# Optimization experiments

Measured on AMD Instinct MI355X. Metric: run time of the kernel, lower is better.

## Reference

```python
import jax, jax.numpy as jnp
import numpy as np

DECAY = 0.99
EPS = 1e-05


def setup_inputs() -> dict:
    key = jax.random.key(0)
    k1, k2, k3 = jax.random.split(key, 3)
    N, K, D = 131072, 1024, 64
    return {
        "z": jax.random.normal(k1, (N, D), dtype=jnp.float32),
        "embeddings": jax.random.normal(k2, (K, D), dtype=jnp.float32),
        "cluster_size": jnp.ones((K,), dtype=jnp.float32),
        "ema_embed_sum": jax.random.normal(k3, (K, D), dtype=jnp.float32),
    }


def reference(z, embeddings, cluster_size, ema_embed_sum):
    # z: [N, D]; embeddings/ema_embed_sum: [K, D]; cluster_size: [K]
    N, D = z.shape
    K = embeddings.shape[0]

    # squared pairwise distances via the ||a||^2 - 2ab + ||b||^2 expansion
    d = (
        jnp.sum(z * z, axis=-1, keepdims=True)
        - 2.0 * (z @ embeddings.T)
        + jnp.sum(embeddings * embeddings, axis=-1)
    )  # [N, K]
    encoding_indices = jnp.argmin(d, axis=1)  # [N]
    z_q = embeddings[encoding_indices]  # [N, D]

    # EMA codebook update (training mode; one_hot.sum(0) == counts, one_hot.T @ z == segment_sum)
    counts = jax.ops.segment_sum(jnp.ones((N,), z.dtype), encoding_indices, num_segments=K)
    new_cluster_size = cluster_size * DECAY + (1.0 - DECAY) * counts
    embed_sum = jax.ops.segment_sum(z, encoding_indices, num_segments=K)  # [K, D]
    new_ema_embed_sum = ema_embed_sum * DECAY + (1.0 - DECAY) * embed_sum
    n = jnp.sum(new_cluster_size)
    cs = (new_cluster_size + EPS) / (n + K * EPS) * n
    new_embeddings = new_ema_embed_sum / cs[:, None]

    commitment_loss = jnp.mean((z - z_q) ** 2)
    z_q_st = z + jax.lax.stop_gradient(z_q - z)  # value == z_q
    return (z_q_st, commitment_loss, encoding_indices, new_embeddings, new_cluster_size, new_ema_embed_sum)
```

## Files before the change

kernel.cpp:

```cpp
#include <hip/hip_runtime.h>

#define N_PTS 131072
#define K_CODES 1024
#define DIM 64
#define DECAYF 0.99f
#define OMDF 0.01f
#define EPSF 1e-5f

#define OUT_ZQ      0
#define OUT_LOSS    8388608
#define OUT_IDX     8388609
#define OUT_NEWEMB  8519681
#define OUT_NEWCS   8585217
#define OUT_NEWEMA  8586241

#define WS_C8       0
#define WS_ACNT     8192
#define WS_LOSS     8208
#define WS_EMBSUM   8224
#define WS_ZERO_END 73760
#define WS_ENORM    73760
#define WS_CUR8     74784
#define WS_CS       82976
#define WS_AMBIG    84000
#define WS_ORDER    215072
#define WS_E2S      215072

#define STEP_BYTES  16640
#define STEP_SHORTS 8320
#define STEP_FLOATS 4160

typedef __attribute__((ext_vector_type(8))) short bf16x8;
typedef __attribute__((ext_vector_type(4))) float f32x4;

static __device__ inline short f2bf(float f) {
    unsigned u = __float_as_uint(f);
    unsigned r = (u + 0x7fffu + ((u >> 16) & 1u)) >> 16;
    return (short)r;
}
static __device__ inline float bf2f(short h) {
    return __uint_as_float(((unsigned)(unsigned short)h) << 16);
}

static __device__ __forceinline__ void gload16(const char* g, char* l) {
    __builtin_amdgcn_global_load_lds(
        (const __attribute__((address_space(1))) void*)g,
        (__attribute__((address_space(3))) void*)l, 16, 0, 0);
}
static __device__ __forceinline__ void gload4(const char* g, char* l) {
    __builtin_amdgcn_global_load_lds(
        (const __attribute__((address_space(1))) void*)g,
        (__attribute__((address_space(3))) void*)l, 4, 0, 0);
}

__global__ __launch_bounds__(256) void econv_kernel(const float* __restrict__ E,
                                                    short* __restrict__ E2S,
                                                    float* __restrict__ enorm) {
    int tid = threadIdx.x;
    int code = blockIdx.x * 64 + (tid >> 2);
    int seg = tid & 3;
    const float4* e4 = (const float4*)(E + (size_t)code * DIM + seg * 16);
    float4 v0 = e4[0], v1 = e4[1], v2 = e4[2], v3 = e4[3];
    float f[16];
    f[0]=v0.x; f[1]=v0.y; f[2]=v0.z; f[3]=v0.w;
    f[4]=v1.x; f[5]=v1.y; f[6]=v1.z; f[7]=v1.w;
    f[8]=v2.x; f[9]=v2.y; f[10]=v2.z; f[11]=v2.w;
    f[12]=v3.x; f[13]=v3.y; f[14]=v3.z; f[15]=v3.w;
    float s = 0.f;
#pragma unroll
    for (int j = 0; j < 16; ++j) s += f[j] * f[j];
    s += __shfl_xor(s, 1);
    s += __shfl_xor(s, 2);
    short hi[16], lo[16];
#pragma unroll
    for (int j = 0; j < 16; ++j) {
        float m = -2.f * f[j];
        short h = f2bf(m);
        hi[j] = h;
        lo[j] = f2bf(m - bf2f(h));
    }
    int sstep = code >> 6;
    int tau = (code >> 4) & 3;
    int cc = code & 15;
    size_t stepb = (size_t)sstep * STEP_SHORTS;
    int p_hi = seg >> 1, p_lo = 2 + (seg >> 1);
#pragma unroll
    for (int h8 = 0; h8 < 2; ++h8) {
        int qq = ((seg & 1) << 1) | h8;
        size_t base = stepb + tau * 2048 + qq * 128 + cc * 8;
        bf16x8 vh, vl;
#pragma unroll
        for (int j = 0; j < 8; ++j) { vh[j] = hi[h8 * 8 + j]; vl[j] = lo[h8 * 8 + j]; }
        *(bf16x8*)(E2S + base + p_hi * 512) = vh;
        *(bf16x8*)(E2S + base + p_lo * 512) = vl;
    }
    if (seg == 0) {
        ((float*)E2S)[(size_t)sstep * STEP_FLOATS + 4096 + tau * 16 + cc] = s;
        enorm[code] = s;
    }
}

__global__ __launch_bounds__(256) void argmin_mfma(const float* __restrict__ z,
                                                   const short* __restrict__ E2S,
                                                   float* __restrict__ out_idx_f,
                                                   float* __restrict__ counts8,
                                                   int* __restrict__ ambig_cnt,
                                                   int* __restrict__ ambig,
                                                   float* __restrict__ loss_ws) {
    int tid = threadIdx.x;
    int w = tid >> 6, lane = tid & 63;
    int c = lane & 15, q = lane >> 4;
    int mbase = blockIdx.x * 256 + w * 64;

    __shared__ char smem[2 * STEP_BYTES] __attribute__((aligned(16)));
    const char* E2Sc = (const char*)E2S;

#define STAGE(SBUF, SSTEP) do {                                               \
    const char* g_ = E2Sc + (size_t)(SSTEP) * STEP_BYTES + w * 1024 + lane * 16; \
    char* l_ = smem + (SBUF) * STEP_BYTES + w * 1024;                         \
    gload16(g_,          l_);                                                 \
    gload16(g_ + 4096,   l_ + 4096);                                          \
    gload16(g_ + 8192,   l_ + 8192);                                          \
    gload16(g_ + 12288,  l_ + 12288);                                         \
    if (w == 0)                                                               \
        gload4(E2Sc + (size_t)(SSTEP) * STEP_BYTES + 16384 + lane * 4,        \
               smem + (SBUF) * STEP_BYTES + 16384);                           \
} while (0)

    STAGE(0, 0);

    bf16x8 a[4][4];
    float znorm_t[4];
#pragma unroll
    for (int t = 0; t < 4; ++t) {
        const float* zp = z + (size_t)(mbase + t * 16 + c) * DIM;
        const float4* z4a = (const float4*)(zp + q * 8);
        const float4* z4b = (const float4*)(zp + 32 + q * 8);
        float f[16];
        float4 v0 = z4a[0], v1 = z4a[1], v2 = z4b[0], v3 = z4b[1];
        f[0]=v0.x; f[1]=v0.y; f[2]=v0.z; f[3]=v0.w;
        f[4]=v1.x; f[5]=v1.y; f[6]=v1.z; f[7]=v1.w;
        f[8]=v2.x; f[9]=v2.y; f[10]=v2.z; f[11]=v2.w;
        f[12]=v3.x; f[13]=v3.y; f[14]=v3.z; f[15]=v3.w;
        float zn = 0.f;
#pragma unroll
        for (int j = 0; j < 16; ++j) zn += f[j] * f[j];
#pragma unroll
        for (int off = 16; off < 64; off <<= 1) zn += __shfl_xor(zn, off);
        znorm_t[t] = zn;
#pragma unroll
        for (int j = 0; j < 8; ++j) {
            short h0 = f2bf(f[j]);
            a[t][0][j] = h0;
            a[t][2][j] = f2bf(f[j] - bf2f(h0));
            short h1 = f2bf(f[8 + j]);
            a[t][1][j] = h1;
            a[t][3][j] = f2bf(f[8 + j] - bf2f(h1));
        }
    }

    float s1[16], s2[16];
#pragma unroll
    for (int idx = 0; idx < 16; ++idx) { s1[idx] = INFINITY; s2[idx] = INFINITY; }

    __syncthreads();

    int bfr = (q << 4) + c;
    for (int st = 0; st < 16; ++st) {
        if (st < 15) STAGE((st + 1) & 1, st + 1);
        const short* lb = (const short*)(smem + (st & 1) * STEP_BYTES);
        const float* lef = (const float*)(smem + (st & 1) * STEP_BYTES + 16384);
#pragma unroll
        for (int tau = 0; tau < 4; ++tau) {
            const bf16x8* bp = (const bf16x8*)lb + tau * 256 + bfr;
            bf16x8 bh0 = bp[0], bh1 = bp[64], bl0 = bp[128], bl1 = bp[192];
            float en = lef[tau * 16 + c];
            unsigned vcode = (unsigned)((((st << 2) + tau) << 4) | c);
#pragma unroll
            for (int t = 0; t < 4; ++t) {
                f32x4 acc = {en, en, en, en};
                acc = __builtin_amdgcn_mfma_f32_16x16x32_bf16(a[t][0], bl0, acc, 0, 0, 0);
                acc = __builtin_amdgcn_mfma_f32_16x16x32_bf16(a[t][1], bl1, acc, 0, 0, 0);
                acc = __builtin_amdgcn_mfma_f32_16x16x32_bf16(a[t][2], bh0, acc, 0, 0, 0);
                acc = __builtin_amdgcn_mfma_f32_16x16x32_bf16(a[t][3], bh1, acc, 0, 0, 0);
                acc = __builtin_amdgcn_mfma_f32_16x16x32_bf16(a[t][0], bh0, acc, 0, 0, 0);
                acc = __builtin_amdgcn_mfma_f32_16x16x32_bf16(a[t][1], bh1, acc, 0, 0, 0);
#pragma unroll
                for (int i = 0; i < 4; ++i) {
                    float sp = __uint_as_float(
                        (__float_as_uint(acc[i]) & 0xFFFFFC00u) | vcode);
                    int idx = t * 4 + i;
                    float ns2 = __builtin_amdgcn_fmed3f(s1[idx], s2[idx], sp);
                    s1[idx] = fminf(s1[idx], sp);
                    s2[idx] = ns2;
                }
            }
        }
        __syncthreads();
    }
#undef STAGE

#pragma unroll
    for (int off = 1; off < 16; off <<= 1) {
#pragma unroll
        for (int idx = 0; idx < 16; ++idx) {
            float os1 = __shfl_xor(s1[idx], off);
            float os2 = __shfl_xor(s2[idx], off);
            float ns1 = fminf(s1[idx], os1);
            s2[idx] = fminf(fmaxf(s1[idx], os1), fminf(s2[idx], os2));
            s1[idx] = ns1;
        }
    }

    float znr[16];
#pragma unroll
    for (int t = 0; t < 4; ++t)
#pragma unroll
        for (int i = 0; i < 4; ++i)
            znr[t * 4 + i] = __shfl(znorm_t[t], (q << 4) | (q * 4 + i), 64);

    __shared__ float lred[16];
    float lsum = 0.f;
    if (c == 0) {
#pragma unroll
        for (int idx = 0; idx < 16; ++idx) {
            int t = idx >> 2, i = idx & 3;
            int row = mbase + t * 16 + q * 4 + i;
            unsigned b1 = __float_as_uint(s1[idx]);
            int code = (int)(b1 & 1023u);
            out_idx_f[row] = (float)code;
            float s1v = __uint_as_float(b1 & 0xFFFFFC00u);
            float gap = s2[idx] - s1[idx];
            float tau = 0.008f + 8e-4f * (fabsf(s1[idx]) + fabsf(s2[idx]));
            if (gap >= tau) {
                atomicAdd(&counts8[(((unsigned)row >> 8) & 7) * K_CODES + code], 1.0f);
                lsum += znr[idx] + s1v;
            } else {
                int p = atomicAdd(ambig_cnt, 1);
                ambig[p] = row;
            }
        }
        lred[w * 4 + q] = lsum;
    }
    __syncthreads();
    if (tid == 0) {
        float tot = 0.f;
#pragma unroll
        for (int i = 0; i < 16; ++i) tot += lred[i];
        atomicAdd(loss_ws, tot);
    }
}

__global__ __launch_bounds__(256) void rescue_kernel(const float* __restrict__ z,
                                                     const float* __restrict__ E,
                                                     const float* __restrict__ enorm,
                                                     const int* __restrict__ ambig_cnt,
                                                     const int* __restrict__ ambig,
                                                     float* __restrict__ out_idx_f,
                                                     float* __restrict__ counts8,
                                                     float* __restrict__ loss_ws) {
    int lane = threadIdx.x & 63;
    int wave = (blockIdx.x * 256 + threadIdx.x) >> 6;
    int nw = gridDim.x * 4;
    int cnt = *ambig_cnt;
    for (int a = 2 * wave; a < cnt; a += 2 * nw) {
        int row0 = ambig[a];
        bool two = (a + 1) < cnt;
        int row1 = two ? ambig[a + 1] : row0;
        const float4* zp0 = (const float4*)(z + (size_t)row0 * DIM);
        const float4* zp1 = (const float4*)(z + (size_t)row1 * DIM);
        float4 zr0[16], zr1[16];
        float zn0 = 0.f, zn1 = 0.f;
#pragma unroll
        for (int i = 0; i < 16; ++i) {
            float4 u = zp0[i], v = zp1[i];
            zr0[i] = u; zr1[i] = v;
            zn0 += u.x * u.x + u.y * u.y + u.z * u.z + u.w * u.w;
            zn1 += v.x * v.x + v.y * v.y + v.z * v.z + v.w * v.w;
        }
        float best0 = INFINITY, best1 = INFINITY;
        int bi0 = 0, bi1 = 0;
        for (int j = 0; j < 16; ++j) {
            int code = j * 64 + lane;
            const float4* ep = (const float4*)(E + (size_t)code * DIM);
            float a0 = 0.f, a1 = 0.f, a2 = 0.f, a3 = 0.f;
            float c0 = 0.f, c1 = 0.f, c2 = 0.f, c3 = 0.f;
#pragma unroll
            for (int i = 0; i < 16; ++i) {
                float4 ev = ep[i];
                a0 += zr0[i].x * ev.x; a1 += zr0[i].y * ev.y;
                a2 += zr0[i].z * ev.z; a3 += zr0[i].w * ev.w;
                c0 += zr1[i].x * ev.x; c1 += zr1[i].y * ev.y;
                c2 += zr1[i].z * ev.z; c3 += zr1[i].w * ev.w;
            }
            float en = enorm[code];
            float s0 = en - 2.f * ((a0 + a1) + (a2 + a3));
            float s1 = en - 2.f * ((c0 + c1) + (c2 + c3));
            if (s0 < best0) { best0 = s0; bi0 = code; }
            if (s1 < best1) { best1 = s1; bi1 = code; }
        }
#pragma unroll
        for (int off = 1; off < 64; off <<= 1) {
            float ob = __shfl_xor(best0, off);
            int oi = __shfl_xor(bi0, off);
            if (ob < best0 || (ob == best0 && oi < bi0)) { best0 = ob; bi0 = oi; }
            float ob1 = __shfl_xor(best1, off);
            int oi1 = __shfl_xor(bi1, off);
            if (ob1 < best1 || (ob1 == best1 && oi1 < bi1)) { best1 = ob1; bi1 = oi1; }
        }
        if (lane == 0) {
            out_idx_f[row0] = (float)bi0;
            atomicAdd(&counts8[(((unsigned)row0 >> 8) & 7) * K_CODES + bi0], 1.0f);
            float ladd = zn0 + best0;
            if (two) {
                out_idx_f[row1] = (float)bi1;
                atomicAdd(&counts8[(((unsigned)row1 >> 8) & 7) * K_CODES + bi1], 1.0f);
                ladd += zn1 + best1;
            }
            atomicAdd(loss_ws, ladd);
        }
    }
}

__global__ __launch_bounds__(1024) void scan_kernel(const float* __restrict__ cluster_size,
                                                    const float* __restrict__ counts8,
                                                    float* __restrict__ ncs_out,
                                                    float* __restrict__ cs_ws,
                                                    int* __restrict__ cursor8) {
    int k = threadIdx.x;
    int lane = k & 63, wv = k >> 6;
    float c8[8];
    float cnt = 0.f;
#pragma unroll
    for (int s = 0; s < 8; ++s) { c8[s] = counts8[s * K_CODES + k]; cnt += c8[s]; }
    float ncs = cluster_size[k] * DECAYF + OMDF * cnt;
    ncs_out[k] = ncs;

    int v = (int)cnt;
    int vs = v;
#pragma unroll
    for (int off = 1; off < 64; off <<= 1) {
        int o = __shfl_up(vs, off, 64);
        if (lane >= off) vs += o;
    }
    float fs = ncs;
#pragma unroll
    for (int off = 1; off < 64; off <<= 1) fs += __shfl_xor(fs, off);

    __shared__ int wtot[16];
    __shared__ float ftot[16];
    __shared__ float nsh;
    if (lane == 63) wtot[wv] = vs;
    if (lane == 0) ftot[wv] = fs;
    __syncthreads();
    if (k == 0) {
        int run = 0; float fn = 0.f;
#pragma unroll
        for (int i = 0; i < 16; ++i) {
            int t = wtot[i]; wtot[i] = run; run += t;
            fn += ftot[i];
        }
        nsh = fn;
    }
    __syncthreads();
    float n = nsh;
    cs_ws[k] = (ncs + EPSF) / (n + (float)K_CODES * EPSF) * n;

    int excl = vs - v + wtot[wv];
    int run = excl;
#pragma unroll
    for (int s = 0; s < 8; ++s) { cursor8[s * K_CODES + k] = run; run += (int)c8[s]; }
}

__global__ __launch_bounds__(256) void scatter_zq_kernel(const float* __restrict__ E,
                                                         const float* __restrict__ idx_f,
                                                         int* __restrict__ cursor8,
                                                         int* __restrict__ order,
                                                         float* __restrict__ zq) {
    __shared__ int s_k[256];
    int tid = threadIdx.x;
    int rbase = blockIdx.x * 256;
    int row = rbase + tid;
    int k = (int)idx_f[row];
    s_k[tid] = k;
    int shard = ((unsigned)row >> 8) & 7;
    int p = atomicAdd(&cursor8[shard * K_CODES + k], 1);
    order[p] = (k << 17) | row;
    __syncthreads();
    size_t ebase = (size_t)rbase * DIM;
#pragma unroll 4
    for (int it = 0; it < 64; ++it) {
        int le = it * 256 + tid;
        int rl = le >> 6, d = le & 63;
        zq[ebase + le] = E[(size_t)s_k[rl] * DIM + d];
    }
}

__global__ __launch_bounds__(256) void segsum_kernel(const float* __restrict__ z,
                                                     const int* __restrict__ order,
                                                     float* __restrict__ embsum) {
    int lane = threadIdx.x & 63;
    int w = threadIdx.x >> 6;
    int wave = blockIdx.x * 4 + w;
    int base = wave * 64;

    int my = order[base + lane];

    int cur = __shfl(my, 0, 64) >> 17;
    float sum = 0.f;
#pragma unroll 8
    for (int i = 0; i < 64; ++i) {
        int p = __shfl(my, i, 64);
        int row = p & 0x1FFFF;
        int code = p >> 17;
        float v = z[(size_t)row * DIM + lane];
        if (code != cur) {
            atomicAdd(&embsum[(size_t)cur * DIM + lane], sum);
            sum = 0.f;
            cur = code;
        }
        sum += v;
    }
    atomicAdd(&embsum[(size_t)cur * DIM + lane], sum);
}

__global__ __launch_bounds__(256) void ema2_kernel(const float* __restrict__ ema,
                                                   const float* __restrict__ embsum,
                                                   const float* __restrict__ cs_ws,
                                                   const float* __restrict__ loss_ws,
                                                   float* __restrict__ newema_out,
                                                   float* __restrict__ newemb_out,
                                                   float* __restrict__ loss_out) {
    int i = blockIdx.x * 256 + threadIdx.x;
    float nes = ema[i] * DECAYF + OMDF * embsum[i];
    newema_out[i] = nes;
    newemb_out[i] = nes / cs_ws[i >> 6];
    if (i == 0)
        loss_out[0] = loss_ws[0] * (1.0f / ((float)N_PTS * (float)DIM));
}

extern "C" void kernel_launch(void* const* d_in, const int* in_sizes, int n_in,
                              void* d_out, int out_size, void* d_ws, size_t ws_size,
                              hipStream_t stream) {
    const float* z            = (const float*)d_in[0];
    const float* E            = (const float*)d_in[1];
    const float* cluster_size = (const float*)d_in[2];
    const float* ema          = (const float*)d_in[3];
    float* out = (float*)d_out;
    float* ws  = (float*)d_ws;

    hipMemsetAsync(ws, 0, (size_t)WS_ZERO_END * sizeof(float), stream);

    econv_kernel<<<K_CODES / 64, 256, 0, stream>>>(E, (short*)(ws + WS_E2S),
                                                   ws + WS_ENORM);

    argmin_mfma<<<N_PTS / 256, 256, 0, stream>>>(z, (const short*)(ws + WS_E2S),
                                                 out + OUT_IDX,
                                                 ws + WS_C8,
                                                 (int*)(ws + WS_ACNT),
                                                 (int*)(ws + WS_AMBIG),
                                                 ws + WS_LOSS);

    rescue_kernel<<<512, 256, 0, stream>>>(z, E, ws + WS_ENORM,
                                           (const int*)(ws + WS_ACNT),
                                           (const int*)(ws + WS_AMBIG),
                                           out + OUT_IDX,
                                           ws + WS_C8,
                                           ws + WS_LOSS);

    scan_kernel<<<1, 1024, 0, stream>>>(cluster_size, ws + WS_C8,
                                        out + OUT_NEWCS, ws + WS_CS,
                                        (int*)(ws + WS_CUR8));

    scatter_zq_kernel<<<N_PTS / 256, 256, 0, stream>>>(E, out + OUT_IDX,
                                                       (int*)(ws + WS_CUR8),
                                                       (int*)(ws + WS_ORDER),
                                                       out + OUT_ZQ);

    segsum_kernel<<<N_PTS / 256, 256, 0, stream>>>(z,
                                                   (const int*)(ws + WS_ORDER),
                                                   ws + WS_EMBSUM);

    ema2_kernel<<<K_CODES * DIM / 256, 256, 0, stream>>>(ema, ws + WS_EMBSUM,
                                                         ws + WS_CS,
                                                         ws + WS_LOSS,
                                                         out + OUT_NEWEMA,
                                                         out + OUT_NEWEMB,
                                                         out + OUT_LOSS);
}
```

Before: 224.3 us.

## Fuse tail kernels into one persistent kernel with grid barriers

Merges the rescue, scan, z_q scatter, segment-sum and EMA kernels into a single persistent launch of 256 blocks that separates its phases with software grid barriers. The workspace memset moves into the codebook conversion kernel, and the argmin kernel's reduction buffer now reuses existing shared memory. The aim is to remove several launches and their gaps on the stream. In exchange, the scatter and segsum phases run on fewer blocks with grid-stride loops, and the spin barrier relies on all 256 blocks being resident at once.

```diff
diff --git a/kernel.cpp b/kernel.cpp
--- a/kernel.cpp
+++ b/kernel.cpp
@@ -6,6 +6,8 @@
 #define DECAYF 0.99f
 #define OMDF 0.01f
 #define EPSF 1e-5f
+
+#define TAIL_BLKS 256
 
 #define OUT_ZQ      0
 #define OUT_LOSS    8388608
@@ -54,9 +56,13 @@
 }
 
 __global__ __launch_bounds__(256) void econv_kernel(const float* __restrict__ E,
-                                                    short* __restrict__ E2S,
-                                                    float* __restrict__ enorm) {
+                                                    float* __restrict__ ws) {
     int tid = threadIdx.x;
+    int gid = blockIdx.x * 256 + tid;
+    for (int i = gid; i < WS_ZERO_END; i += 16 * 256) ws[i] = 0.f;
+
+    short* E2S = (short*)(ws + WS_E2S);
+    float* enorm = ws + WS_ENORM;
     int code = blockIdx.x * 64 + (tid >> 2);
     int seg = tid & 3;
     const float4* e4 = (const float4*)(E + (size_t)code * DIM + seg * 16);
@@ -219,7 +225,7 @@
         for (int i = 0; i < 4; ++i)
             znr[t * 4 + i] = __shfl(znorm_t[t], (q << 4) | (q * 4 + i), 64);
 
-    __shared__ float lred[16];
+    float* lred = (float*)smem;
     float lsum = 0.f;
     if (c == 0) {
 #pragma unroll
@@ -251,192 +257,216 @@
     }
 }
 
-__global__ __launch_bounds__(256) void rescue_kernel(const float* __restrict__ z,
-                                                     const float* __restrict__ E,
-                                                     const float* __restrict__ enorm,
-                                                     const int* __restrict__ ambig_cnt,
-                                                     const int* __restrict__ ambig,
-                                                     float* __restrict__ out_idx_f,
-                                                     float* __restrict__ counts8,
-                                                     float* __restrict__ loss_ws) {
-    int lane = threadIdx.x & 63;
-    int wave = (blockIdx.x * 256 + threadIdx.x) >> 6;
-    int nw = gridDim.x * 4;
-    int cnt = *ambig_cnt;
-    for (int a = 2 * wave; a < cnt; a += 2 * nw) {
-        int row0 = ambig[a];
-        bool two = (a + 1) < cnt;
-        int row1 = two ? ambig[a + 1] : row0;
-        const float4* zp0 = (const float4*)(z + (size_t)row0 * DIM);
-        const float4* zp1 = (const float4*)(z + (size_t)row1 * DIM);
-        float4 zr0[16], zr1[16];
-        float zn0 = 0.f, zn1 = 0.f;
-#pragma unroll
-        for (int i = 0; i < 16; ++i) {
-            float4 u = zp0[i], v = zp1[i];
-            zr0[i] = u; zr1[i] = v;
-            zn0 += u.x * u.x + u.y * u.y + u.z * u.z + u.w * u.w;
-            zn1 += v.x * v.x + v.y * v.y + v.z * v.z + v.w * v.w;
-        }
-        float best0 = INFINITY, best1 = INFINITY;
-        int bi0 = 0, bi1 = 0;
-        for (int j = 0; j < 16; ++j) {
-            int code = j * 64 + lane;
-            const float4* ep = (const float4*)(E + (size_t)code * DIM);
-            float a0 = 0.f, a1 = 0.f, a2 = 0.f, a3 = 0.f;
-            float c0 = 0.f, c1 = 0.f, c2 = 0.f, c3 = 0.f;
+static __device__ __forceinline__ void gbar(int* bar_cnt, int* bar_gen, int nblk) {
+    __syncthreads();
+    if (threadIdx.x == 0) {
+        __threadfence();
+        int g = atomicAdd(bar_gen, 0);
+        if (atomicAdd(bar_cnt, 1) == nblk - 1) {
+            atomicExch(bar_cnt, 0);
+            __threadfence();
+            atomicAdd(bar_gen, 1);
+        } else {
+            while (atomicAdd(bar_gen, 0) == g) __builtin_amdgcn_s_sleep(8);
+        }
+        __threadfence();
+    }
+    __syncthreads();
+}
+
+__global__ __launch_bounds__(256) void vq_tail(const float* __restrict__ z,
+                                               const float* __restrict__ E,
+                                               const float* __restrict__ cluster_size,
+                                               const float* __restrict__ ema,
+                                               float* __restrict__ out,
+                                               float* __restrict__ ws) {
+    float* out_idx_f = out + OUT_IDX;
+    float* zq        = out + OUT_ZQ;
+    float* counts8   = ws + WS_C8;
+    int*   acnt16    = (int*)(ws + WS_ACNT);
+    float* loss_ws   = ws + WS_LOSS;
+    float* embsum    = ws + WS_EMBSUM;
+    float* enorm     = ws + WS_ENORM;
+    int*   cursor8   = (int*)(ws + WS_CUR8);
+    float* cs_ws     = ws + WS_CS;
+    int*   ambig     = (int*)(ws + WS_AMBIG);
+    int*   order     = (int*)(ws + WS_ORDER);
+    int*   bar_cnt   = acnt16 + 8;
+    int*   bar_gen   = acnt16 + 9;
+
+    __shared__ int s_k[256];
+    __shared__ int wtot[4];
+    __shared__ float ftot[4];
+    __shared__ float nsh;
+
+    int tid = threadIdx.x;
+    int bid = blockIdx.x;
+    int gtid = bid * 256 + tid;
+    int lane = tid & 63;
+    int w = tid >> 6;
+
+    {
+        int wave = gtid >> 6;
+        int nw = gridDim.x * 4;
+        int cnt = acnt16[0];
+        for (int a = 2 * wave; a < cnt; a += 2 * nw) {
+            int row0 = ambig[a];
+            bool two = (a + 1) < cnt;
+            int row1 = two ? ambig[a + 1] : row0;
+            const float4* zp0 = (const float4*)(z + (size_t)row0 * DIM);
+            const float4* zp1 = (const float4*)(z + (size_t)row1 * DIM);
+            float4 zr0[16], zr1[16];
+            float zn0 = 0.f, zn1 = 0.f;
 #pragma unroll
             for (int i = 0; i < 16; ++i) {
-                float4 ev = ep[i];
-                a0 += zr0[i].x * ev.x; a1 += zr0[i].y * ev.y;
-                a2 += zr0[i].z * ev.z; a3 += zr0[i].w * ev.w;
-                c0 += zr1[i].x * ev.x; c1 += zr1[i].y * ev.y;
-                c2 += zr1[i].z * ev.z; c3 += zr1[i].w * ev.w;
-            }
-            float en = enorm[code];
-            float s0 = en - 2.f * ((a0 + a1) + (a2 + a3));
-            float s1 = en - 2.f * ((c0 + c1) + (c2 + c3));
-            if (s0 < best0) { best0 = s0; bi0 = code; }
-            if (s1 < best1) { best1 = s1; bi1 = code; }
-        }
+                float4 u = zp0[i], v = zp1[i];
+                zr0[i] = u; zr1[i] = v;
+                zn0 += u.x * u.x + u.y * u.y + u.z * u.z + u.w * u.w;
+                zn1 += v.x * v.x + v.y * v.y + v.z * v.z + v.w * v.w;
+            }
+            float best0 = INFINITY, best1 = INFINITY;
+            int bi0 = 0, bi1 = 0;
+            for (int j = 0; j < 16; ++j) {
+                int code = j * 64 + lane;
+                const float4* ep = (const float4*)(E + (size_t)code * DIM);
+                float a0 = 0.f, a1 = 0.f, a2 = 0.f, a3 = 0.f;
+                float c0 = 0.f, c1 = 0.f, c2 = 0.f, c3 = 0.f;
+#pragma unroll
+                for (int i = 0; i < 16; ++i) {
+                    float4 ev = ep[i];
+                    a0 += zr0[i].x * ev.x; a1 += zr0[i].y * ev.y;
+                    a2 += zr0[i].z * ev.z; a3 += zr0[i].w * ev.w;
+                    c0 += zr1[i].x * ev.x; c1 += zr1[i].y * ev.y;
+                    c2 += zr1[i].z * ev.z; c3 += zr1[i].w * ev.w;
+                }
+                float en = enorm[code];
+                float s0 = en - 2.f * ((a0 + a1) + (a2 + a3));
+                float s1 = en - 2.f * ((c0 + c1) + (c2 + c3));
+                if (s0 < best0) { best0 = s0; bi0 = code; }
+                if (s1 < best1) { best1 = s1; bi1 = code; }
+            }
+#pragma unroll
+            for (int off = 1; off < 64; off <<= 1) {
+                float ob = __shfl_xor(best0, off);
+                int oi = __shfl_xor(bi0, off);
+                if (ob < best0 || (ob == best0 && oi < bi0)) { best0 = ob; bi0 = oi; }
+                float ob1 = __shfl_xor(best1, off);
+                int oi1 = __shfl_xor(bi1, off);
+                if (ob1 < best1 || (ob1 == best1 && oi1 < bi1)) { best1 = ob1; bi1 = oi1; }
+            }
+            if (lane == 0) {
+                out_idx_f[row0] = (float)bi0;
+                atomicAdd(&counts8[(((unsigned)row0 >> 8) & 7) * K_CODES + bi0], 1.0f);
+                float ladd = zn0 + best0;
+                if (two) {
+                    out_idx_f[row1] = (float)bi1;
+                    atomicAdd(&counts8[(((unsigned)row1 >> 8) & 7) * K_CODES + bi1], 1.0f);
+                    ladd += zn1 + best1;
+                }
+                atomicAdd(loss_ws, ladd);
+            }
+        }
+    }
+    gbar(bar_cnt, bar_gen, TAIL_BLKS);
+
+    if (bid == 0) {
+        int wv = tid >> 6;
+        float c8v[4][8];
+        float ncs4[4];
+        int tsum = 0; float fsum = 0.f;
+#pragma unroll
+        for (int u = 0; u < 4; ++u) {
+            int kk = tid * 4 + u;
+            float cnt = 0.f;
+#pragma unroll
+            for (int s = 0; s < 8; ++s) { c8v[u][s] = counts8[s * K_CODES + kk]; cnt += c8v[u][s]; }
+            float ncs = cluster_size[kk] * DECAYF + OMDF * cnt;
+            (out + OUT_NEWCS)[kk] = ncs;
+            ncs4[u] = ncs;
+            tsum += (int)cnt;
+            fsum += ncs;
+        }
+        int vs = tsum;
 #pragma unroll
         for (int off = 1; off < 64; off <<= 1) {
-            float ob = __shfl_xor(best0, off);
-            int oi = __shfl_xor(bi0, off);
-            if (ob < best0 || (ob == best0 && oi < bi0)) { best0 = ob; bi0 = oi; }
-            float ob1 = __shfl_xor(best1, off);
-            int oi1 = __shfl_xor(bi1, off);
-            if (ob1 < best1 || (ob1 == best1 && oi1 < bi1)) { best1 = ob1; bi1 = oi1; }
-        }
-        if (lane == 0) {
-            out_idx_f[row0] = (float)bi0;
-            atomicAdd(&counts8[(((unsigned)row0 >> 8) & 7) * K_CODES + bi0], 1.0f);
-            float ladd = zn0 + best0;
-            if (two) {
-                out_idx_f[row1] = (float)bi1;
-                atomicAdd(&counts8[(((unsigned)row1 >> 8) & 7) * K_CODES + bi1], 1.0f);
-                ladd += zn1 + best1;
-            }
-            atomicAdd(loss_ws, ladd);
-        }
-    }
-}
-
-__global__ __launch_bounds__(1024) void scan_kernel(const float* __restrict__ cluster_size,
-                                                    const float* __restrict__ counts8,
-                                                    float* __restrict__ ncs_out,
-                                                    float* __restrict__ cs_ws,
-                                                    int* __restrict__ cursor8) {
-    int k = threadIdx.x;
-    int lane = k & 63, wv = k >> 6;
-    float c8[8];
-    float cnt = 0.f;
-#pragma unroll
-    for (int s = 0; s < 8; ++s) { c8[s] = counts8[s * K_CODES + k]; cnt += c8[s]; }
-    float ncs = cluster_size[k] * DECAYF + OMDF * cnt;
-    ncs_out[k] = ncs;
-
-    int v = (int)cnt;
-    int vs = v;
-#pragma unroll
-    for (int off = 1; off < 64; off <<= 1) {
-        int o = __shfl_up(vs, off, 64);
-        if (lane >= off) vs += o;
-    }
-    float fs = ncs;
-#pragma unroll
-    for (int off = 1; off < 64; off <<= 1) fs += __shfl_xor(fs, off);
-
-    __shared__ int wtot[16];
-    __shared__ float ftot[16];
-    __shared__ float nsh;
-    if (lane == 63) wtot[wv] = vs;
-    if (lane == 0) ftot[wv] = fs;
-    __syncthreads();
-    if (k == 0) {
-        int run = 0; float fn = 0.f;
-#pragma unroll
-        for (int i = 0; i < 16; ++i) {
-            int t = wtot[i]; wtot[i] = run; run += t;
-            fn += ftot[i];
-        }
-        nsh = fn;
-    }
-    __syncthreads();
-    float n = nsh;
-    cs_ws[k] = (ncs + EPSF) / (n + (float)K_CODES * EPSF) * n;
-
-    int excl = vs - v + wtot[wv];
-    int run = excl;
-#pragma unroll
-    for (int s = 0; s < 8; ++s) { cursor8[s * K_CODES + k] = run; run += (int)c8[s]; }
-}
-
-__global__ __launch_bounds__(256) void scatter_zq_kernel(const float* __restrict__ E,
-                                                         const float* __restrict__ idx_f,
-                                                         int* __restrict__ cursor8,
-                                                         int* __restrict__ order,
-                                                         float* __restrict__ zq) {
-    __shared__ int s_k[256];
-    int tid = threadIdx.x;
-    int rbase = blockIdx.x * 256;
-    int row = rbase + tid;
-    int k = (int)idx_f[row];
-    s_k[tid] = k;
-    int shard = ((unsigned)row >> 8) & 7;
-    int p = atomicAdd(&cursor8[shard * K_CODES + k], 1);
-    order[p] = (k << 17) | row;
-    __syncthreads();
-    size_t ebase = (size_t)rbase * DIM;
+            int o = __shfl_up(vs, off, 64);
+            if (lane >= off) vs += o;
+        }
+        float fs = fsum;
+#pragma unroll
+        for (int off = 1; off < 64; off <<= 1) fs += __shfl_xor(fs, off);
+        if (lane == 63) wtot[wv] = vs;
+        if (lane == 0) ftot[wv] = fs;
+        __syncthreads();
+        if (tid == 0) {
+            int run = 0; float fn = 0.f;
+#pragma unroll
+            for (int i = 0; i < 4; ++i) { int x = wtot[i]; wtot[i] = run; run += x; fn += ftot[i]; }
+            nsh = fn;
+        }
+        __syncthreads();
+        float n = nsh;
+        int run = (vs - tsum) + wtot[wv];
+#pragma unroll
+        for (int u = 0; u < 4; ++u) {
+            int kk = tid * 4 + u;
+            cs_ws[kk] = (ncs4[u] + EPSF) / (n + (float)K_CODES * EPSF) * n;
+#pragma unroll
+            for (int s = 0; s < 8; ++s) { cursor8[s * K_CODES + kk] = run; run += (int)c8v[u][s]; }
+        }
+    }
+    gbar(bar_cnt, bar_gen, TAIL_BLKS);
+
+    for (int rb = bid; rb < N_PTS / 256; rb += gridDim.x) {
+        int rbase = rb * 256;
+        int row = rbase + tid;
+        int k = (int)out_idx_f[row];
+        s_k[tid] = k;
+        int shard = ((unsigned)row >> 8) & 7;
+        int p = atomicAdd(&cursor8[shard * K_CODES + k], 1);
+        order[p] = (k << 17) | row;
+        __syncthreads();
+        size_t ebase = (size_t)rbase * DIM;
 #pragma unroll 4
-    for (int it = 0; it < 64; ++it) {
-        int le = it * 256 + tid;
-        int rl = le >> 6, d = le & 63;
-        zq[ebase + le] = E[(size_t)s_k[rl] * DIM + d];
-    }
-}
-
-__global__ __launch_bounds__(256) void segsum_kernel(const float* __restrict__ z,
-                                                     const int* __restrict__ order,
-                                                     float* __restrict__ embsum) {
-    int lane = threadIdx.x & 63;
-    int w = threadIdx.x >> 6;
-    int wave = blockIdx.x * 4 + w;
-    int base = wave * 64;
-
-    int my = order[base + lane];
-
-    int cur = __shfl(my, 0, 64) >> 17;
-    float sum = 0.f;
+        for (int it = 0; it < 64; ++it) {
+            int le = it * 256 + tid;
+            int rl = le >> 6, d = le & 63;
+            zq[ebase + le] = E[(size_t)s_k[rl] * DIM + d];
+        }
+        __syncthreads();
+    }
+    gbar(bar_cnt, bar_gen, TAIL_BLKS);
+
+    for (int vb = bid; vb < N_PTS / 256; vb += gridDim.x) {
+        int wave = vb * 4 + w;
+        int base = wave * 64;
+        int my = order[base + lane];
+        int cur = __shfl(my, 0, 64) >> 17;
+        float sum = 0.f;
 #pragma unroll 8
-    for (int i = 0; i < 64; ++i) {
-        int p = __shfl(my, i, 64);
-        int row = p & 0x1FFFF;
-        int code = p >> 17;
-        float v = z[(size_t)row * DIM + lane];
-        if (code != cur) {
-            atomicAdd(&embsum[(size_t)cur * DIM + lane], sum);
-            sum = 0.f;
-            cur = code;
-        }
-        sum += v;
-    }
-    atomicAdd(&embsum[(size_t)cur * DIM + lane], sum);
-}
-
-__global__ __launch_bounds__(256) void ema2_kernel(const float* __restrict__ ema,
-                                                   const float* __restrict__ embsum,
-                                                   const float* __restrict__ cs_ws,
-                                                   const float* __restrict__ loss_ws,
-                                                   float* __restrict__ newema_out,
-                                                   float* __restrict__ newemb_out,
-                                                   float* __restrict__ loss_out) {
-    int i = blockIdx.x * 256 + threadIdx.x;
-    float nes = ema[i] * DECAYF + OMDF * embsum[i];
-    newema_out[i] = nes;
-    newemb_out[i] = nes / cs_ws[i >> 6];
-    if (i == 0)
-        loss_out[0] = loss_ws[0] * (1.0f / ((float)N_PTS * (float)DIM));
+        for (int i = 0; i < 64; ++i) {
+            int p = __shfl(my, i, 64);
+            int row = p & 0x1FFFF;
+            int code = p >> 17;
+            float v = z[(size_t)row * DIM + lane];
+            if (code != cur) {
+                atomicAdd(&embsum[(size_t)cur * DIM + lane], sum);
+                sum = 0.f;
+                cur = code;
+            }
+            sum += v;
+        }
+        atomicAdd(&embsum[(size_t)cur * DIM + lane], sum);
+    }
+    gbar(bar_cnt, bar_gen, TAIL_BLKS);
+
+    for (int i = gtid; i < K_CODES * DIM; i += gridDim.x * 256) {
+        float nes = ema[i] * DECAYF + OMDF * embsum[i];
+        (out + OUT_NEWEMA)[i] = nes;
+        (out + OUT_NEWEMB)[i] = nes / cs_ws[i >> 6];
+    }
+    if (gtid == 0)
+        (out + OUT_LOSS)[0] = loss_ws[0] * (1.0f / ((float)N_PTS * (float)DIM));
 }
 
 extern "C" void kernel_launch(void* const* d_in, const int* in_sizes, int n_in,
@@ -449,10 +479,7 @@
     float* out = (float*)d_out;
     float* ws  = (float*)d_ws;
 
-    hipMemsetAsync(ws, 0, (size_t)WS_ZERO_END * sizeof(float), stream);
-
-    econv_kernel<<<K_CODES / 64, 256, 0, stream>>>(E, (short*)(ws + WS_E2S),
-                                                   ws + WS_ENORM);
+    econv_kernel<<<K_CODES / 64, 256, 0, stream>>>(E, ws);
 
     argmin_mfma<<<N_PTS / 256, 256, 0, stream>>>(z, (const short*)(ws + WS_E2S),
                                                  out + OUT_IDX,
@@ -461,30 +488,5 @@
                                                  (int*)(ws + WS_AMBIG),
                                                  ws + WS_LOSS);
 
-    rescue_kernel<<<512, 256, 0, stream>>>(z, E, ws + WS_ENORM,
-                                           (const int*)(ws + WS_ACNT),
-                                           (const int*)(ws + WS_AMBIG),
-                                           out + OUT_IDX,
-                                           ws + WS_C8,
-                                           ws + WS_LOSS);
-
-    scan_kernel<<<1, 1024, 0, stream>>>(cluster_size, ws + WS_C8,
-                                        out + OUT_NEWCS, ws + WS_CS,
-                                        (int*)(ws + WS_CUR8));
-
-    scatter_zq_kernel<<<N_PTS / 256, 256, 0, stream>>>(E, out + OUT_IDX,
-                                                       (int*)(ws + WS_CUR8),
-                                                       (int*)(ws + WS_ORDER),
-                                                       out + OUT_ZQ);
-
-    segsum_kernel<<<N_PTS / 256, 256, 0, stream>>>(z,
-                                                   (const int*)(ws + WS_ORDER),
-                                                   ws + WS_EMBSUM);
-
-    ema2_kernel<<<K_CODES * DIM / 256, 256, 0, stream>>>(ema, ws + WS_EMBSUM,
-                                                         ws + WS_CS,
-                                                         ws + WS_LOSS,
-                                                         out + OUT_NEWEMA,
-                                                         out + OUT_NEWEMB,
-                                                         out + OUT_LOSS);
-}
+    vq_tail<<<TAIL_BLKS, 256, 0, stream>>>(z, E, cluster_size, ema, out, ws);
+}
```

Measured after the change: 320.9 us. 43.1% more time.

## Replace sort-based segment sum with direct atomics fused with z_q gather

Applied to the files above, without the earlier changes.

Drops the counting-sort pipeline (scan for cursors, scatter into an order array, segmented reduction) and instead has each row atomically add its z values straight into the code's embedding sum, fused with the z_q gather in one kernel. The cluster-size and normaliser computation moves into an extra block of that kernel, and workspace zeroing moves from a memset into econv_kernel. This removes two launches and the order-array round trip, but can cause heavy per-element atomic contention on popular codes. It also makes the float summation order nondeterministic.

```diff
diff --git a/kernel.cpp b/kernel.cpp
--- a/kernel.cpp
+++ b/kernel.cpp
@@ -20,10 +20,8 @@
 #define WS_EMBSUM   8224
 #define WS_ZERO_END 73760
 #define WS_ENORM    73760
-#define WS_CUR8     74784
 #define WS_CS       82976
 #define WS_AMBIG    84000
-#define WS_ORDER    215072
 #define WS_E2S      215072
 
 #define STEP_BYTES  16640
@@ -54,9 +52,13 @@
 }
 
 __global__ __launch_bounds__(256) void econv_kernel(const float* __restrict__ E,
-                                                    short* __restrict__ E2S,
-                                                    float* __restrict__ enorm) {
+                                                    float* __restrict__ ws) {
     int tid = threadIdx.x;
+    int gid = blockIdx.x * 256 + tid;
+    for (int i = gid; i < WS_ZERO_END; i += 16 * 256) ws[i] = 0.f;
+
+    short* E2S = (short*)(ws + WS_E2S);
+    float* enorm = ws + WS_ENORM;
     int code = blockIdx.x * 64 + (tid >> 2);
     int seg = tid & 3;
     const float4* e4 = (const float4*)(E + (size_t)code * DIM + seg * 16);
@@ -219,7 +221,7 @@
         for (int i = 0; i < 4; ++i)
             znr[t * 4 + i] = __shfl(znorm_t[t], (q << 4) | (q * 4 + i), 64);
 
-    __shared__ float lred[16];
+    float* lred = (float*)smem;
     float lsum = 0.f;
     if (c == 0) {
 #pragma unroll
@@ -322,106 +324,65 @@
     }
 }
 
-__global__ __launch_bounds__(1024) void scan_kernel(const float* __restrict__ cluster_size,
-                                                    const float* __restrict__ counts8,
-                                                    float* __restrict__ ncs_out,
-                                                    float* __restrict__ cs_ws,
-                                                    int* __restrict__ cursor8) {
-    int k = threadIdx.x;
-    int lane = k & 63, wv = k >> 6;
-    float c8[8];
-    float cnt = 0.f;
-#pragma unroll
-    for (int s = 0; s < 8; ++s) { c8[s] = counts8[s * K_CODES + k]; cnt += c8[s]; }
-    float ncs = cluster_size[k] * DECAYF + OMDF * cnt;
-    ncs_out[k] = ncs;
-
-    int v = (int)cnt;
-    int vs = v;
-#pragma unroll
-    for (int off = 1; off < 64; off <<= 1) {
-        int o = __shfl_up(vs, off, 64);
-        if (lane >= off) vs += o;
-    }
-    float fs = ncs;
-#pragma unroll
-    for (int off = 1; off < 64; off <<= 1) fs += __shfl_xor(fs, off);
-
-    __shared__ int wtot[16];
-    __shared__ float ftot[16];
+__global__ __launch_bounds__(256) void zq_embsum_kernel(const float* __restrict__ z,
+                                                        const float* __restrict__ E,
+                                                        const float* __restrict__ idx_f,
+                                                        const float* __restrict__ cluster_size,
+                                                        const float* __restrict__ counts8,
+                                                        float* __restrict__ ncs_out,
+                                                        float* __restrict__ cs_ws,
+                                                        float* __restrict__ embsum,
+                                                        float* __restrict__ zq) {
+    __shared__ int s_k[64];
+    __shared__ float ftot[4];
     __shared__ float nsh;
-    if (lane == 63) wtot[wv] = vs;
-    if (lane == 0) ftot[wv] = fs;
+
+    int tid = threadIdx.x;
+    int bid = blockIdx.x;
+    int lane = tid & 63;
+    int w = tid >> 6;
+
+    if (bid == 2048) {
+        float ncs4[4];
+        float fsum = 0.f;
+#pragma unroll
+        for (int u = 0; u < 4; ++u) {
+            int kk = tid * 4 + u;
+            float cnt = 0.f;
+#pragma unroll
+            for (int s = 0; s < 8; ++s) cnt += counts8[s * K_CODES + kk];
+            float ncs = cluster_size[kk] * DECAYF + OMDF * cnt;
+            ncs_out[kk] = ncs;
+            ncs4[u] = ncs;
+            fsum += ncs;
+        }
+#pragma unroll
+        for (int off = 1; off < 64; off <<= 1) fsum += __shfl_xor(fsum, off);
+        if (lane == 0) ftot[w] = fsum;
+        __syncthreads();
+        if (tid == 0) nsh = ftot[0] + ftot[1] + ftot[2] + ftot[3];
+        __syncthreads();
+        float n = nsh;
+#pragma unroll
+        for (int u = 0; u < 4; ++u) {
+            int kk = tid * 4 + u;
+            cs_ws[kk] = (ncs4[u] + EPSF) / (n + (float)K_CODES * EPSF) * n;
+        }
+        return;
+    }
+
+    int rbase = bid * 64;
+    if (tid < 64) s_k[tid] = (int)idx_f[rbase + tid];
     __syncthreads();
-    if (k == 0) {
-        int run = 0; float fn = 0.f;
-#pragma unroll
-        for (int i = 0; i < 16; ++i) {
-            int t = wtot[i]; wtot[i] = run; run += t;
-            fn += ftot[i];
-        }
-        nsh = fn;
-    }
-    __syncthreads();
-    float n = nsh;
-    cs_ws[k] = (ncs + EPSF) / (n + (float)K_CODES * EPSF) * n;
-
-    int excl = vs - v + wtot[wv];
-    int run = excl;
-#pragma unroll
-    for (int s = 0; s < 8; ++s) { cursor8[s * K_CODES + k] = run; run += (int)c8[s]; }
-}
-
-__global__ __launch_bounds__(256) void scatter_zq_kernel(const float* __restrict__ E,
-                                                         const float* __restrict__ idx_f,
-                                                         int* __restrict__ cursor8,
-                                                         int* __restrict__ order,
-                                                         float* __restrict__ zq) {
-    __shared__ int s_k[256];
-    int tid = threadIdx.x;
-    int rbase = blockIdx.x * 256;
-    int row = rbase + tid;
-    int k = (int)idx_f[row];
-    s_k[tid] = k;
-    int shard = ((unsigned)row >> 8) & 7;
-    int p = atomicAdd(&cursor8[shard * K_CODES + k], 1);
-    order[p] = (k << 17) | row;
-    __syncthreads();
-    size_t ebase = (size_t)rbase * DIM;
+
 #pragma unroll 4
-    for (int it = 0; it < 64; ++it) {
-        int le = it * 256 + tid;
-        int rl = le >> 6, d = le & 63;
-        zq[ebase + le] = E[(size_t)s_k[rl] * DIM + d];
-    }
-}
-
-__global__ __launch_bounds__(256) void segsum_kernel(const float* __restrict__ z,
-                                                     const int* __restrict__ order,
-                                                     float* __restrict__ embsum) {
-    int lane = threadIdx.x & 63;
-    int w = threadIdx.x >> 6;
-    int wave = blockIdx.x * 4 + w;
-    int base = wave * 64;
-
-    int my = order[base + lane];
-
-    int cur = __shfl(my, 0, 64) >> 17;
-    float sum = 0.f;
-#pragma unroll 8
-    for (int i = 0; i < 64; ++i) {
-        int p = __shfl(my, i, 64);
-        int row = p & 0x1FFFF;
-        int code = p >> 17;
-        float v = z[(size_t)row * DIM + lane];
-        if (code != cur) {
-            atomicAdd(&embsum[(size_t)cur * DIM + lane], sum);
-            sum = 0.f;
-            cur = code;
-        }
-        sum += v;
-    }
-    atomicAdd(&embsum[(size_t)cur * DIM + lane], sum);
+    for (int r = w; r < 64; r += 4) {
+        int row = rbase + r;
+        int k = s_k[r];
+        float zv = z[(size_t)row * DIM + lane];
+        atomicAdd(&embsum[(size_t)k * DIM + lane], zv);
+        zq[(size_t)row * DIM + lane] = E[(size_t)k * DIM + lane];
+    }
 }
 
 __global__ __launch_bounds__(256) void ema2_kernel(const float* __restrict__ ema,
@@ -449,10 +410,7 @@
     float* out = (float*)d_out;
     float* ws  = (float*)d_ws;
 
-    hipMemsetAsync(ws, 0, (size_t)WS_ZERO_END * sizeof(float), stream);
-
-    econv_kernel<<<K_CODES / 64, 256, 0, stream>>>(E, (short*)(ws + WS_E2S),
-                                                   ws + WS_ENORM);
+    econv_kernel<<<K_CODES / 64, 256, 0, stream>>>(E, ws);
 
     argmin_mfma<<<N_PTS / 256, 256, 0, stream>>>(z, (const short*)(ws + WS_E2S),
                                                  out + OUT_IDX,
@@ -468,18 +426,13 @@
                                            ws + WS_C8,
                                            ws + WS_LOSS);
 
-    scan_kernel<<<1, 1024, 0, stream>>>(cluster_size, ws + WS_C8,
-                                        out + OUT_NEWCS, ws + WS_CS,
-                                        (int*)(ws + WS_CUR8));
-
-    scatter_zq_kernel<<<N_PTS / 256, 256, 0, stream>>>(E, out + OUT_IDX,
-                                                       (int*)(ws + WS_CUR8),
-                                                       (int*)(ws + WS_ORDER),
-                                                       out + OUT_ZQ);
-
-    segsum_kernel<<<N_PTS / 256, 256, 0, stream>>>(z,
-                                                   (const int*)(ws + WS_ORDER),
-                                                   ws + WS_EMBSUM);
+    zq_embsum_kernel<<<N_PTS / 64 + 1, 256, 0, stream>>>(z, E, out + OUT_IDX,
+                                                         cluster_size,
+                                                         ws + WS_C8,
+                                                         out + OUT_NEWCS,
+                                                         ws + WS_CS,
+                                                         ws + WS_EMBSUM,
+                                                         out + OUT_ZQ);
 
     ema2_kernel<<<K_CODES * DIM / 256, 256, 0, stream>>>(ema, ws + WS_EMBSUM,
                                                          ws + WS_CS,
```

Measured after the change: 247.6 us. 10.4% more time.
